# Kernel tuning notes

Hardware: AMD Instinct MI355X
Metric: run time of the kernel (lower is better)

The kernel has to match this reference:

```python
import jax, jax.numpy as jnp
import numpy as np

# dims: B batch, N seq, D model_dim, R lora rank, C codebooks, K codebook_input_channel, P kv pairs, M per-codebook output
B, N, D, R, C, K, P = 4, 2048, 1024, 8, 64, 16, 64
M = (D * R) // C  # 128


def setup_inputs() -> dict:
    key = jax.random.key(0)
    ks = jax.random.split(key, 7)
    x = jax.random.normal(ks[0], (B, N, D), dtype=jnp.float32)
    W_A = jax.random.normal(ks[1], (C, K, D), dtype=jnp.float32) * (D ** -0.5)
    emb_A = jax.random.uniform(ks[2], (C, P, K), dtype=jnp.float32, minval=-1.5, maxval=1.5)
    vals_A = jax.random.normal(ks[3], (C, P, M), dtype=jnp.float32)
    W_B = jax.random.normal(ks[4], (C, K, D), dtype=jnp.float32) * (D ** -0.5)
    emb_B = jax.random.uniform(ks[5], (C, P, K), dtype=jnp.float32, minval=-1.5, maxval=1.5)
    vals_B = jax.random.normal(ks[6], (C, P, M), dtype=jnp.float32)
    return {"x": x, "W_A": W_A, "emb_A": emb_A, "vals_A": vals_A,
            "W_B": W_B, "emb_B": emb_B, "vals_B": vals_B}


def _discrete_kv(x, W, emb, vals):
    # x: [B,N,D]; W: [C,K,D] (Linear weight per codebook); emb: [C,P,K]; vals: [C,P,M]
    proj = jnp.einsum('bnd,ckd->cbnk', x, W)  # per-codebook linear projection
    # squared euclidean distance to each key (argmin is same as cdist argmin)
    d2 = (jnp.sum(proj * proj, axis=-1, keepdims=True)
          - 2.0 * jnp.einsum('cbnk,cpk->cbnp', proj, emb)
          + jnp.sum(emb * emb, axis=-1)[:, None, None, :])  # [C,B,N,P]
    idx = jnp.argmin(d2, axis=-1)                      # [C,B,N]
    y = jax.vmap(lambda v, i: v[i])(vals, idx)          # [C,B,N,M]
    # concat over codebooks on last dim -> [B,N,C*M], then view as [B,N,R,D]
    return jnp.transpose(y, (1, 2, 0, 3)).reshape(x.shape[0], x.shape[1], R, D)


def reference(x, W_A, emb_A, vals_A, W_B, emb_B, vals_B):
    A = _discrete_kv(x, W_A, emb_A, vals_A)   # [B,N,R,D]
    Bm = _discrete_kv(x, W_B, emb_B, vals_B)  # [B,N,R,D]
    t = jnp.einsum('bnd,bnrd->bnr', x, A)
    return jnp.einsum('bnr,bnrd->bnd', t, Bm)
```

## Files before the change

kernel.cpp:

```cpp
#include <hip/hip_runtime.h>

#define NTOK   8192
#define DMODEL 1024
#define NC     64
#define NK     16
#define NP     64
#define NM     128
#define LCAP   (1 << 18)
#define MARGIN 2e-3f

typedef _Float16 f16x8  __attribute__((ext_vector_type(8)));
typedef float    f32x16 __attribute__((ext_vector_type(16)));

#define AS1 __attribute__((address_space(1)))
#define AS3 __attribute__((address_space(3)))

__device__ __forceinline__ void glds16(const void* g, void* l) {
    __builtin_amdgcn_global_load_lds((const AS1 void*)g, (AS3 void*)l, 16, 0, 0);
}

__global__ __launch_bounds__(256) void k_split(
    const float* __restrict__ x, const float* __restrict__ W_A, const float* __restrict__ W_B,
    short* __restrict__ xh, short* __restrict__ xl,
    short* __restrict__ whA, short* __restrict__ wlA,
    short* __restrict__ whB, short* __restrict__ wlB)
{
    const int t = blockIdx.x * 256 + threadIdx.x;
    const int NX = 128 * NTOK;
    const int NW = 128 * 1024;

    const float* src;
    short *dh, *dl;
    if (t < NX) {
        const int chunk = t >> 13, tok = t & 8191;
        src = x + (size_t)tok * DMODEL + chunk * 8;
        dh = xh + (size_t)t * 8;  dl = xl + (size_t)t * 8;
    } else if (t < NX + NW) {
        const int u = t - NX, chunk = u >> 10, ck = u & 1023;
        src = W_A + (size_t)ck * DMODEL + chunk * 8;
        dh = whA + (size_t)u * 8; dl = wlA + (size_t)u * 8;
    } else {
        const int u = t - NX - NW, chunk = u >> 10, ck = u & 1023;
        src = W_B + (size_t)ck * DMODEL + chunk * 8;
        dh = whB + (size_t)u * 8; dl = wlB + (size_t)u * 8;
    }

    const float4 a = *(const float4*)src;
    const float4 b = *(const float4*)(src + 4);
    const float v[8] = {a.x, a.y, a.z, a.w, b.x, b.y, b.z, b.w};
    unsigned h[8], l[8];
    #pragma unroll
    for (int j = 0; j < 8; ++j) {
        const _Float16 hf = (_Float16)v[j];
        const _Float16 lf = (_Float16)(v[j] - (float)hf);
        h[j] = (unsigned)__builtin_bit_cast(unsigned short, hf);
        l[j] = (unsigned)__builtin_bit_cast(unsigned short, lf);
    }
    *(int4*)dh = make_int4((int)(h[0] | (h[1] << 16)), (int)(h[2] | (h[3] << 16)),
                           (int)(h[4] | (h[5] << 16)), (int)(h[6] | (h[7] << 16)));
    *(int4*)dl = make_int4((int)(l[0] | (l[1] << 16)), (int)(l[2] | (l[3] << 16)),
                           (int)(l[4] | (l[5] << 16)), (int)(l[6] | (l[7] << 16)));
}

struct Frags { f16x8 ah[4], al[4], bh[2], bl[2]; };

__device__ __forceinline__ void load_frags(Frags& f, const short* bb,
                                           int aoff, int boff) {
    #pragma unroll
    for (int m = 0; m < 4; ++m) {
        f.ah[m] = *(const f16x8*)(bb + aoff + m * 256);
        f.al[m] = *(const f16x8*)(bb + 4096 + aoff + m * 256);
    }
    #pragma unroll
    for (int n = 0; n < 2; ++n) {
        f.bh[n] = *(const f16x8*)(bb + boff + n * 256);
        f.bl[n] = *(const f16x8*)(bb + 4096 + boff + n * 256);
    }
}

__device__ __forceinline__ void do_mfma(f32x16 acc[4][2], const Frags& f) {
    #pragma unroll
    for (int m = 0; m < 4; ++m)
        #pragma unroll
        for (int n = 0; n < 2; ++n)
            acc[m][n] = __builtin_amdgcn_mfma_f32_32x32x16_f16(f.ah[m], f.bh[n], acc[m][n], 0, 0, 0);
    #pragma unroll
    for (int m = 0; m < 4; ++m)
        #pragma unroll
        for (int n = 0; n < 2; ++n)
            acc[m][n] = __builtin_amdgcn_mfma_f32_32x32x16_f16(f.ah[m], f.bl[n], acc[m][n], 0, 0, 0);
    #pragma unroll
    for (int m = 0; m < 4; ++m)
        #pragma unroll
        for (int n = 0; n < 2; ++n)
            acc[m][n] = __builtin_amdgcn_mfma_f32_32x32x16_f16(f.al[m], f.bh[n], acc[m][n], 0, 0, 0);
}

__global__ __launch_bounds__(512, 1) void k_mfma_argmin(
    const short* __restrict__ xh, const short* __restrict__ xl,
    const short* __restrict__ whA, const short* __restrict__ wlA,
    const short* __restrict__ whB, const short* __restrict__ wlB,
    const float* __restrict__ emb_A, const float* __restrict__ emb_B,
    int* __restrict__ idxbuf, int* __restrict__ list, int* __restrict__ cnt)
{
    __shared__ __align__(16) float smem[32768];
    short* ls = (short*)smem;
    float* projT = smem;
    float* embS  = smem + 16640;
    float* e2S   = smem + 24832;

    const int tid = threadIdx.x;
    const int bid = blockIdx.x;
    const int swz = (bid & 7) * 32 + (bid >> 3);
    const int tb  = swz >> 3;
    const int ot  = swz & 7;
    const int set = ot >> 2;
    const short* __restrict__ wh = set ? whB : whA;
    const short* __restrict__ wl = set ? wlB : wlA;
    const float* __restrict__ Ep = set ? emb_B : emb_A;
    const int ckbase = (ot & 3) * 256;

    const int lane = tid & 63;
    const int wid  = tid >> 6;
    const int wr   = wid >> 2;
    const int wc   = wid & 3;
    const int lr31 = lane & 31;
    const int lk2  = lane >> 5;

    f32x16 acc[4][2];
    #pragma unroll
    for (int m = 0; m < 4; ++m)
        #pragma unroll
        for (int n = 0; n < 2; ++n)
            #pragma unroll
            for (int r = 0; r < 16; ++r) acc[m][n][r] = 0.f;

    const size_t oA = ((size_t)(tid >> 8) * NTOK + tb * 256 + (tid & 255)) * 8;
    const size_t oB = ((size_t)(tid >> 8) * 1024 + ckbase + (tid & 255)) * 8;

    #define STAGE(buf, st)                                                   \
        do {                                                                 \
            const size_t sa_ = (size_t)(st) * (size_t)(2 * NTOK * 8);        \
            const size_t sb_ = (size_t)(st) * (size_t)(2 * 1024 * 8);        \
            short* lb_ = ls + (buf) * 16384 + tid * 8;                       \
            glds16(xh + oA + sa_, lb_);                                      \
            glds16(xl + oA + sa_, lb_ + 4096);                               \
            glds16(wh + oB + sb_, lb_ + 8192);                               \
            glds16(wl + oB + sb_, lb_ + 12288);                              \
        } while (0)

    const int aoff = (lk2 * 256 + wr * 128 + lr31) * 8;
    const int boff = 8192 + (lk2 * 256 + wc * 64 + lr31) * 8;

    Frags fE, fO;

    STAGE(0, 0);
    STAGE(1, 1);
    STAGE(2, 2);
    STAGE(3, 3);
    asm volatile("s_waitcnt vmcnt(12)" ::: "memory");
    __builtin_amdgcn_s_barrier();
    __builtin_amdgcn_sched_barrier(0);
    load_frags(fE, ls, aoff, boff);

    #define BODY(T, CUR, NXT)                                                \
        do {                                                                 \
            asm volatile("s_waitcnt vmcnt(8)" ::: "memory");                 \
            asm volatile("s_waitcnt lgkmcnt(0)" ::: "memory");               \
            __builtin_amdgcn_sched_barrier(0);                               \
            __builtin_amdgcn_s_barrier();                                    \
            __builtin_amdgcn_sched_barrier(0);                               \
            load_frags(NXT, ls + (((T) + 1) & 3) * 16384, aoff, boff);       \
            { const int ts_ = ((T) + 4 < 64) ? (T) + 4 : 63;                 \
              STAGE((T) & 3, ts_); }                                         \
            __builtin_amdgcn_s_setprio(1);                                   \
            do_mfma(acc, CUR);                                               \
            __builtin_amdgcn_s_setprio(0);                                   \
        } while (0)

    for (int t = 0; t < 62; t += 2) {
        BODY(t, fE, fO);
        BODY(t + 1, fO, fE);
    }
    BODY(62, fE, fO);
    asm volatile("s_waitcnt lgkmcnt(0)" ::: "memory");
    __builtin_amdgcn_sched_barrier(0);
    __builtin_amdgcn_s_barrier();
    __builtin_amdgcn_s_setprio(1);
    do_mfma(acc, fO);
    __builtin_amdgcn_s_setprio(0);
    #undef BODY
    #undef STAGE

    asm volatile("s_waitcnt vmcnt(0)" ::: "memory");
    __builtin_amdgcn_s_barrier();

    #pragma unroll
    for (int ch = 0; ch < 2; ++ch) {
        __syncthreads();
        {
            const float4* eg = (const float4*)(Ep + (size_t)((ot & 3) * 16 + ch * 8) * NP * NK);
            float4* es = (float4*)embS;
            #pragma unroll
            for (int i = 0; i < 4; ++i) es[tid + 512 * i] = eg[tid + 512 * i];
        }
        __syncthreads();
        {
            const float* e = embS + tid * 16;
            float s = 0.f;
            #pragma unroll
            for (int k = 0; k < 16; ++k) s = fmaf(e[k], e[k], s);
            e2S[tid] = s;
        }
        #pragma unroll
        for (int c = 0; c < 4; ++c) {
            __syncthreads();
            if (wr == (c >> 1)) {
                #pragma unroll
                for (int mi = 0; mi < 2; ++mi) {
                    const int m = (c & 1) * 2 + mi;
                    #pragma unroll
                    for (int n = 0; n < 2; ++n) {
                        const int col = wc * 64 + n * 32 + lr31;
                        #pragma unroll
                        for (int r = 0; r < 16; ++r) {
                            const int trow = mi * 32 + (r & 3) + 8 * (r >> 2) + 4 * lk2;
                            projT[col * 65 + trow] = acc[m][n][r];
                        }
                    }
                }
            }
            __syncthreads();
            {
                const int lt = tid & 63, cbl = tid >> 6;
                float pr[16];
                #pragma unroll
                for (int k = 0; k < 16; ++k)
                    pr[k] = projT[((ch * 8 + cbl) * 16 + k) * 65 + lt];
                const float4* eb4 = (const float4*)(embS + cbl * 1024);
                const float* e2 = e2S + cbl * 64;
                float best = 1e30f, second = 1e30f;
                int bp = 0;
                #pragma unroll 4
                for (int p = 0; p < 64; ++p) {
                    const float4 e0 = eb4[p * 4 + 0], e1 = eb4[p * 4 + 1];
                    const float4 e2v = eb4[p * 4 + 2], e3 = eb4[p * 4 + 3];
                    float s = 0.f;
                    s = fmaf(pr[0], e0.x, s);   s = fmaf(pr[1], e0.y, s);
                    s = fmaf(pr[2], e0.z, s);   s = fmaf(pr[3], e0.w, s);
                    s = fmaf(pr[4], e1.x, s);   s = fmaf(pr[5], e1.y, s);
                    s = fmaf(pr[6], e1.z, s);   s = fmaf(pr[7], e1.w, s);
                    s = fmaf(pr[8], e2v.x, s);  s = fmaf(pr[9], e2v.y, s);
                    s = fmaf(pr[10], e2v.z, s); s = fmaf(pr[11], e2v.w, s);
                    s = fmaf(pr[12], e3.x, s);  s = fmaf(pr[13], e3.y, s);
                    s = fmaf(pr[14], e3.z, s);  s = fmaf(pr[15], e3.w, s);
                    const float g = fmaf(-2.f, s, e2[p]);
                    if (g < best) { second = best; best = g; bp = p; }
                    else if (g < second) { second = g; }
                }
                const int cbook = (ot & 3) * 16 + ch * 8 + cbl;
                const int gtok = tb * 256 + c * 64 + lt;
                idxbuf[(set * NC + cbook) * NTOK + gtok] = bp;
                if (second - best < MARGIN) {
                    const int slot = atomicAdd(cnt, 1);
                    if (slot < LCAP) list[slot] = (set << 19) | (cbook << 13) | gtok;
                }
            }
        }
    }
}

__global__ __launch_bounds__(256) void k_refine(
    const float* __restrict__ x,
    const float* __restrict__ W_A, const float* __restrict__ W_B,
    const float* __restrict__ emb_A, const float* __restrict__ emb_B,
    const int* __restrict__ list, const int* __restrict__ cnt,
    int* __restrict__ idxbuf)
{
    int n = *cnt;
    if (n > LCAP) n = LCAP;
    const int lane = threadIdx.x & 63;
    const int wave = (int)((blockIdx.x * blockDim.x + threadIdx.x) >> 6);
    const int nw   = (int)((gridDim.x * blockDim.x) >> 6);

    for (int i = wave; i < n; i += nw) {
        const int code = list[i];
        const int tok = code & 8191;
        const int c   = (code >> 13) & 63;
        const int set = (code >> 19) & 1;
        const float* __restrict__ Wp = set ? W_B : W_A;
        const float* __restrict__ Ep = set ? emb_B : emb_A;

        double pk[16];
        #pragma unroll
        for (int k = 0; k < 16; ++k) pk[k] = 0.0;
        for (int dd = 0; dd < 16; ++dd) {
            const int d = dd * 64 + lane;
            const double xv = (double)x[(size_t)tok * DMODEL + d];
            #pragma unroll
            for (int k = 0; k < 16; ++k)
                pk[k] = fma(xv, (double)Wp[(size_t)(c * 16 + k) * DMODEL + d], pk[k]);
        }
        #pragma unroll
        for (int k = 0; k < 16; ++k) {
            #pragma unroll
            for (int off = 32; off; off >>= 1)
                pk[k] += __shfl_xor(pk[k], off, 64);
        }
        double d2 = 0.0;
        #pragma unroll
        for (int k = 0; k < 16; ++k) {
            const double t = pk[k] - (double)Ep[(size_t)(c * NP + lane) * NK + k];
            d2 = fma(t, t, d2);
        }
        int bp = lane;
        double bv = d2;
        #pragma unroll
        for (int off = 32; off; off >>= 1) {
            const double ov = __shfl_xor(bv, off, 64);
            const int    op = __shfl_xor(bp, off, 64);
            if (ov < bv || (ov == bv && op < bp)) { bv = ov; bp = op; }
        }
        if (lane == 0) idxbuf[(set * NC + c) * NTOK + tok] = bp;
    }
}

__global__ __launch_bounds__(256) void k_combine(
    const float* __restrict__ x,
    const float* __restrict__ vals_A, const float* __restrict__ vals_B,
    const int* __restrict__ idxbuf, float* __restrict__ out)
{
    __shared__ float xsh[1032];
    __shared__ float part[256];
    __shared__ float tsh[8];
    __shared__ int sIA[64];
    __shared__ int sIB[64];

    const int tid = threadIdx.x;
    const int tok = blockIdx.x;

    if (tid < 64) {
        sIA[tid] = idxbuf[tid * NTOK + tok];
        sIB[tid] = idxbuf[(NC + tid) * NTOK + tok];
    }
    {
        const float4 v = *(const float4*)(x + (size_t)tok * DMODEL + tid * 4);
        const int base = tid * 4 + (tid >> 5);
        xsh[base + 0] = v.x;
        xsh[base + 1] = v.y;
        xsh[base + 2] = v.z;
        xsh[base + 3] = v.w;
    }
    __syncthreads();
    {
        const int c = tid & 63, mseg = tid >> 6;
        const int ia = sIA[c];
        const float4* va = (const float4*)(vals_A + (size_t)(c * NP + ia) * NM + mseg * 32);
        const float* xb = xsh + (c & 7) * 129 + mseg * 32;
        float s = 0.f;
        #pragma unroll
        for (int i = 0; i < 8; ++i) {
            const float4 v = va[i];
            s = fmaf(v.x, xb[i * 4 + 0], s);
            s = fmaf(v.y, xb[i * 4 + 1], s);
            s = fmaf(v.z, xb[i * 4 + 2], s);
            s = fmaf(v.w, xb[i * 4 + 3], s);
        }
        part[tid] = s;
    }
    __syncthreads();
    if (tid < 8) {
        float s = 0.f;
        #pragma unroll
        for (int m = 0; m < 4; ++m)
            #pragma unroll
            for (int j = 0; j < 8; ++j)
                s += part[m * 64 + tid * 8 + j];
        tsh[tid] = s;
    }
    __syncthreads();
    {
        const int d0 = tid * 4, dblk = tid >> 5, dm = d0 & 127;
        float o0 = 0.f, o1 = 0.f, o2 = 0.f, o3 = 0.f;
        #pragma unroll
        for (int r = 0; r < 8; ++r) {
            const int cb = 8 * r + dblk;
            const int ib = sIB[cb];
            const float4 v = *(const float4*)(vals_B + (size_t)(cb * NP + ib) * NM + dm);
            const float tv = tsh[r];
            o0 = fmaf(tv, v.x, o0);
            o1 = fmaf(tv, v.y, o1);
            o2 = fmaf(tv, v.z, o2);
            o3 = fmaf(tv, v.w, o3);
        }
        *(float4*)(out + (size_t)tok * DMODEL + d0) = make_float4(o0, o1, o2, o3);
    }
}

extern "C" void kernel_launch(void* const* d_in, const int* in_sizes, int n_in,
                              void* d_out, int out_size, void* d_ws, size_t ws_size,
                              hipStream_t stream)
{
    const float* x      = (const float*)d_in[0];
    const float* W_A    = (const float*)d_in[1];
    const float* emb_A  = (const float*)d_in[2];
    const float* vals_A = (const float*)d_in[3];
    const float* W_B    = (const float*)d_in[4];
    const float* emb_B  = (const float*)d_in[5];
    const float* vals_B = (const float*)d_in[6];
    float* out = (float*)d_out;

    char* w = (char*)d_ws;
    int*   cnt    = (int*)w;
    int*   list   = (int*)(w + 16);
    int*   idxbuf = (int*)(w + 16 + sizeof(int) * (size_t)LCAP);
    size_t off = 16 + sizeof(int) * (size_t)LCAP + sizeof(int) * (size_t)(2 * NC * NTOK);
    short* xh  = (short*)(w + off); off += (size_t)NTOK * DMODEL * 2;
    short* xl  = (short*)(w + off); off += (size_t)NTOK * DMODEL * 2;
    short* whA = (short*)(w + off); off += (size_t)1024 * DMODEL * 2;
    short* wlA = (short*)(w + off); off += (size_t)1024 * DMODEL * 2;
    short* whB = (short*)(w + off); off += (size_t)1024 * DMODEL * 2;
    short* wlB = (short*)(w + off);

    hipMemsetAsync(cnt, 0, sizeof(int), stream);
    k_split<<<5120, 256, 0, stream>>>(x, W_A, W_B, xh, xl, whA, wlA, whB, wlB);
    k_mfma_argmin<<<256, 512, 0, stream>>>(xh, xl, whA, wlA, whB, wlB,
                                           emb_A, emb_B, idxbuf, list, cnt);
    k_refine<<<1024, 256, 0, stream>>>(x, W_A, W_B, emb_A, emb_B, list, cnt, idxbuf);
    k_combine<<<NTOK, 256, 0, stream>>>(x, vals_A, vals_B, idxbuf, out);
}
```

Measured before the change: 240.6 us.

## Compute codebook distances with split-fp16 MFMA instead of scalar FMA loops

Replaces the scalar per-thread distance loop in the argmin epilogue with MFMA matrix ops. Projections are written to LDS as hi/lo fp16 pairs in a swizzled layout, and embeddings are held in registers as scaled hi/lo fp16 fragments, with the squared norms folded in as the accumulator init. The top-2 reduction now runs over MFMA output registers plus a cross-half shuffle. This is meant to cut the VALU cost and the number of barriers in the epilogue. The trade-off is some precision from the 3-term split product and more LDS traffic for the projection write-out.

Result: slower. 298.5 us (+24.1%).

```diff
diff --git a/kernel.cpp b/kernel.cpp
--- a/kernel.cpp
+++ b/kernel.cpp
@@ -105,9 +105,6 @@
 {
     __shared__ __align__(16) float smem[32768];
     short* ls = (short*)smem;
-    float* projT = smem;
-    float* embS  = smem + 16640;
-    float* e2S   = smem + 24832;
 
     const int tid = threadIdx.x;
     const int bid = blockIdx.x;
@@ -124,7 +121,7 @@
     const int wid  = tid >> 6;
     const int wr   = wid >> 2;
     const int wc   = wid & 3;
-    const int lr31 = lane & 31;
+    const int l31  = lane & 31;
     const int lk2  = lane >> 5;
 
     f32x16 acc[4][2];
@@ -149,8 +146,8 @@
             glds16(wl + oB + sb_, lb_ + 12288);                              \
         } while (0)
 
-    const int aoff = (lk2 * 256 + wr * 128 + lr31) * 8;
-    const int boff = 8192 + (lk2 * 256 + wc * 64 + lr31) * 8;
+    const int aoff = (lk2 * 256 + wr * 128 + l31) * 8;
+    const int boff = 8192 + (lk2 * 256 + wc * 64 + l31) * 8;
 
     Frags fE, fO;
 
@@ -195,75 +192,110 @@
     asm volatile("s_waitcnt vmcnt(0)" ::: "memory");
     __builtin_amdgcn_s_barrier();
 
-    #pragma unroll
-    for (int ch = 0; ch < 2; ++ch) {
+    for (int h = 0; h < 2; ++h) {
+        const int cbH = wid;
+        const int cbG = (ot & 3) * 16 + h * 8 + cbH;
+
+        float ev0[8], ev1[8];
+        {
+            const float4* q0 = (const float4*)(Ep + ((size_t)(cbG * NP + l31) * NK + lk2 * 8));
+            const float4* q1 = (const float4*)(Ep + ((size_t)(cbG * NP + 32 + l31) * NK + lk2 * 8));
+            const float4 a0 = q0[0], b0 = q0[1], a1 = q1[0], b1 = q1[1];
+            ev0[0]=a0.x; ev0[1]=a0.y; ev0[2]=a0.z; ev0[3]=a0.w;
+            ev0[4]=b0.x; ev0[5]=b0.y; ev0[6]=b0.z; ev0[7]=b0.w;
+            ev1[0]=a1.x; ev1[1]=a1.y; ev1[2]=a1.z; ev1[3]=a1.w;
+            ev1[4]=b1.x; ev1[5]=b1.y; ev1[6]=b1.z; ev1[7]=b1.w;
+        }
+        float p20 = 0.f, p21 = 0.f;
+        #pragma unroll
+        for (int j = 0; j < 8; ++j) {
+            p20 = fmaf(ev0[j], ev0[j], p20);
+            p21 = fmaf(ev1[j], ev1[j], p21);
+        }
+        const float e20 = p20 + __shfl_xor(p20, 32);
+        const float e21 = p21 + __shfl_xor(p21, 32);
+        f16x8 A0h, A0l, A1h, A1l;
+        #pragma unroll
+        for (int j = 0; j < 8; ++j) {
+            const float v0 = -2.f * ev0[j];
+            const _Float16 h0 = (_Float16)v0;
+            A0h[j] = h0; A0l[j] = (_Float16)(v0 - (float)h0);
+            const float v1 = -2.f * ev1[j];
+            const _Float16 h1 = (_Float16)v1;
+            A1h[j] = h1; A1l[j] = (_Float16)(v1 - (float)h1);
+        }
+        f32x16 gi0, gi1;
+        #pragma unroll
+        for (int r = 0; r < 16; ++r) {
+            const int cr = (r & 3) + 8 * (r >> 2);
+            gi0[r] = __shfl(e20, cr + 4 * lk2);
+            gi1[r] = __shfl(e21, cr + 4 * lk2);
+        }
+
         __syncthreads();
-        {
-            const float4* eg = (const float4*)(Ep + (size_t)((ot & 3) * 16 + ch * 8) * NP * NK);
-            float4* es = (float4*)embS;
-            #pragma unroll
-            for (int i = 0; i < 4; ++i) es[tid + 512 * i] = eg[tid + 512 * i];
+        if ((wc >> 1) == h) {
+            #pragma unroll
+            for (int m = 0; m < 4; ++m)
+                #pragma unroll
+                for (int n = 0; n < 2; ++n)
+                    #pragma unroll
+                    for (int r = 0; r < 16; ++r) {
+                        const int colh = (wc & 1) * 64 + n * 32 + l31;
+                        const int cb2  = ((colh >> 4) << 1) + ((colh >> 3) & 1);
+                        const int kj   = colh & 7;
+                        const int tok  = wr * 128 + m * 32 + (r & 3) + 8 * (r >> 2) + 4 * lk2;
+                        const int sw   = ((cb2 << 8) + tok) ^ (cb2 & 7);
+                        const float v  = acc[m][n][r];
+                        const _Float16 hf = (_Float16)v;
+                        ls[sw * 8 + kj]         = __builtin_bit_cast(short, hf);
+                        ls[32768 + sw * 8 + kj] = __builtin_bit_cast(short, (_Float16)(v - (float)hf));
+                    }
         }
         __syncthreads();
-        {
-            const float* e = embS + tid * 16;
-            float s = 0.f;
-            #pragma unroll
-            for (int k = 0; k < 16; ++k) s = fmaf(e[k], e[k], s);
-            e2S[tid] = s;
-        }
-        #pragma unroll
-        for (int c = 0; c < 4; ++c) {
-            __syncthreads();
-            if (wr == (c >> 1)) {
-                #pragma unroll
-                for (int mi = 0; mi < 2; ++mi) {
-                    const int m = (c & 1) * 2 + mi;
-                    #pragma unroll
-                    for (int n = 0; n < 2; ++n) {
-                        const int col = wc * 64 + n * 32 + lr31;
-                        #pragma unroll
-                        for (int r = 0; r < 16; ++r) {
-                            const int trow = mi * 32 + (r & 3) + 8 * (r >> 2) + 4 * lk2;
-                            projT[col * 65 + trow] = acc[m][n][r];
-                        }
-                    }
-                }
+
+        for (int grp = 0; grp < 8; ++grp) {
+            const int cb2 = cbH * 2 + lk2;
+            const int sw8 = (((cb2 << 8) + grp * 32 + l31) ^ (cb2 & 7)) * 8;
+            const f16x8 Bh = *(const f16x8*)(ls + sw8);
+            const f16x8 Bl = *(const f16x8*)(ls + 32768 + sw8);
+            f32x16 s0 = gi0, s1 = gi1;
+            s0 = __builtin_amdgcn_mfma_f32_32x32x16_f16(A0h, Bh, s0, 0, 0, 0);
+            s0 = __builtin_amdgcn_mfma_f32_32x32x16_f16(A0h, Bl, s0, 0, 0, 0);
+            s0 = __builtin_amdgcn_mfma_f32_32x32x16_f16(A0l, Bh, s0, 0, 0, 0);
+            s1 = __builtin_amdgcn_mfma_f32_32x32x16_f16(A1h, Bh, s1, 0, 0, 0);
+            s1 = __builtin_amdgcn_mfma_f32_32x32x16_f16(A1h, Bl, s1, 0, 0, 0);
+            s1 = __builtin_amdgcn_mfma_f32_32x32x16_f16(A1l, Bh, s1, 0, 0, 0);
+
+            float best = 1e30f, second = 1e30f;
+            int bp = 0;
+            #pragma unroll
+            for (int r = 0; r < 16; ++r) {
+                const int cr = (r & 3) + 8 * (r >> 2);
+                const float g = s0[r];
+                const int p = cr + 4 * lk2;
+                if (g < best) { second = best; best = g; bp = p; }
+                else if (g < second) { second = g; }
             }
-            __syncthreads();
-            {
-                const int lt = tid & 63, cbl = tid >> 6;
-                float pr[16];
-                #pragma unroll
-                for (int k = 0; k < 16; ++k)
-                    pr[k] = projT[((ch * 8 + cbl) * 16 + k) * 65 + lt];
-                const float4* eb4 = (const float4*)(embS + cbl * 1024);
-                const float* e2 = e2S + cbl * 64;
-                float best = 1e30f, second = 1e30f;
-                int bp = 0;
-                #pragma unroll 4
-                for (int p = 0; p < 64; ++p) {
-                    const float4 e0 = eb4[p * 4 + 0], e1 = eb4[p * 4 + 1];
-                    const float4 e2v = eb4[p * 4 + 2], e3 = eb4[p * 4 + 3];
-                    float s = 0.f;
-                    s = fmaf(pr[0], e0.x, s);   s = fmaf(pr[1], e0.y, s);
-                    s = fmaf(pr[2], e0.z, s);   s = fmaf(pr[3], e0.w, s);
-                    s = fmaf(pr[4], e1.x, s);   s = fmaf(pr[5], e1.y, s);
-                    s = fmaf(pr[6], e1.z, s);   s = fmaf(pr[7], e1.w, s);
-                    s = fmaf(pr[8], e2v.x, s);  s = fmaf(pr[9], e2v.y, s);
-                    s = fmaf(pr[10], e2v.z, s); s = fmaf(pr[11], e2v.w, s);
-                    s = fmaf(pr[12], e3.x, s);  s = fmaf(pr[13], e3.y, s);
-                    s = fmaf(pr[14], e3.z, s);  s = fmaf(pr[15], e3.w, s);
-                    const float g = fmaf(-2.f, s, e2[p]);
-                    if (g < best) { second = best; best = g; bp = p; }
-                    else if (g < second) { second = g; }
-                }
-                const int cbook = (ot & 3) * 16 + ch * 8 + cbl;
-                const int gtok = tb * 256 + c * 64 + lt;
-                idxbuf[(set * NC + cbook) * NTOK + gtok] = bp;
+            #pragma unroll
+            for (int r = 0; r < 16; ++r) {
+                const int cr = (r & 3) + 8 * (r >> 2);
+                const float g = s1[r];
+                const int p = 32 + cr + 4 * lk2;
+                if (g < best) { second = best; best = g; bp = p; }
+                else if (g < second) { second = g; }
+            }
+            const float ob = __shfl_xor(best, 32);
+            const float os = __shfl_xor(second, 32);
+            const int   op = __shfl_xor(bp, 32);
+            if (ob < best) { second = fminf(best, os); best = ob; bp = op; }
+            else           { second = fminf(second, ob); }
+
+            if (lane < 32) {
+                const int tokG = tb * 256 + grp * 32 + lane;
+                idxbuf[(set * NC + cbG) * NTOK + tokG] = bp;
                 if (second - best < MARGIN) {
                     const int slot = atomicAdd(cnt, 1);
-                    if (slot < LCAP) list[slot] = (set << 19) | (cbook << 13) | gtok;
+                    if (slot < LCAP) list[slot] = (set << 19) | (cbG << 13) | tokG;
                 }
             }
         }
```
